# Optimization experiments

Hardware: AMD Instinct MI355X
Metric: run time of the kernel (lower is better)

The kernel has to match this reference:

```python
import jax, jax.numpy as jnp
import numpy as np

# hyperparameters (match init_kwargs)
LS = 0.2; GAMMA = 2.0; THING_W = 2.0; L_DB = 0.1; SIGMA = 0.05; TEMP = 0.1
L_DISTILL = 1.0; L_BPL = 0.5; L_ALIGN = 5.0; L_PROTO = 0.5; L_ENT = 0.3
L_IU = 0.5; L_IB = 0.5
MIN_PIX = 25; NUM_IDS = 24  # instance ids in [0, NUM_IDS)


def setup_inputs() -> dict:
    key = jax.random.key(0)
    k0, k1, k2, k3, k4 = jax.random.split(key, 5)
    B, C, H, W, D = 4, 27, 160, 160, 768
    return {
        "logits": jax.random.normal(k0, (B, C, H, W), jnp.float32),
        "cause_logits": jax.random.normal(k1, (B, C, H, W), jnp.float32),
        "dinov2_features": jax.random.normal(k2, (B, D, H, W), jnp.float32),
        "depth": jax.random.uniform(k3, (B, 1, H, W), jnp.float32),
        "instance_map": jax.random.randint(k4, (B, 1, H, W), 0, NUM_IDS),
    }


def _bce(x, y):
    x = jnp.clip(x, 1e-6, 1.0 - 1e-6)
    return -(y * jnp.log(x) + (1.0 - y) * jnp.log1p(-x)).mean()


def _forward(logits, cause_logits, dinov2_features, depth, instance_map):
    B, C, H, W = logits.shape
    logp = jax.nn.log_softmax(logits, axis=1)
    probs = jnp.exp(logp)

    # ---- distill: label-smoothed CE vs CAUSE hard labels, focal + thing + depth-boundary weights
    cause_labels = jnp.argmax(cause_logits, axis=1)  # (B,H,W)
    nll = -jnp.take_along_axis(logp, cause_labels[:, None], axis=1)[:, 0]  # (B,H,W)
    ce = (1.0 - LS) * nll + LS * (-logp.mean(axis=1))
    pt = jnp.exp(-jax.lax.stop_gradient(ce))
    w = (1.0 - pt) ** GAMMA
    thing = (cause_labels >= 11) & (cause_labels <= 18)
    w = jnp.where(thing, w * THING_W, w)
    gh = jnp.pad(jnp.abs(depth[:, :, 1:, :] - depth[:, :, :-1, :]), ((0, 0), (0, 0), (0, 1), (0, 0)))
    gw = jnp.pad(jnp.abs(depth[:, :, :, 1:] - depth[:, :, :, :-1]), ((0, 0), (0, 0), (0, 0), (0, 1)))
    gmag = (gh + gw)[:, 0]  # (B,H,W)
    gnorm = gmag / (gmag.mean() + 1e-6)
    w = w * (1.0 + L_DB * jnp.minimum(gnorm, 3.0))
    l_distill = (ce * w).mean()

    # ---- boundary preservation loss (CE re-weighted at pseudo-label boundaries)
    pl = jnp.pad(cause_labels, ((0, 0), (1, 1), (1, 1)), mode="edge")
    boundary = ((cause_labels != pl[:, 1:-1, 2:]) | (cause_labels != pl[:, 1:-1, :-2]) |
                (cause_labels != pl[:, 2:, 1:-1]) | (cause_labels != pl[:, :-2, 1:-1])).astype(jnp.float32)
    bsum = boundary.sum()
    l_bpl = jnp.where(bsum > 0, (ce * boundary).sum() / jnp.maximum(bsum, 1.0), 0.0)

    # ---- depth-boundary alignment
    two_s2 = 2.0 * SIGMA ** 2
    ddh = jnp.abs(depth[:, :, :, 1:] - depth[:, :, :, :-1])
    wh = jnp.exp(-(ddh ** 2) / two_s2)
    pdh = ((probs[:, :, :, 1:] - probs[:, :, :, :-1]) ** 2).sum(axis=1, keepdims=True)
    ddv = jnp.abs(depth[:, :, 1:, :] - depth[:, :, :-1, :])
    wv = jnp.exp(-(ddv ** 2) / two_s2)
    pdv = ((probs[:, :, 1:, :] - probs[:, :, :-1, :]) ** 2).sum(axis=1, keepdims=True)
    l_align = (wh * pdh).mean() + (wv * pdv).mean()

    # ---- feature prototype loss
    N = H * W
    probs_t = jax.nn.softmax(logits / TEMP, axis=1).reshape(B, C, N)   # (B,C,N)
    feats = dinov2_features.reshape(B, -1, N)                          # (B,D,N)
    protos = jnp.einsum("bdn,bcn->bdc", feats, probs_t)               # (B,D,C)
    wsum = probs_t.sum(axis=2)[:, None, :]                             # (B,1,C)
    protos = protos / (wsum + 1e-6)
    protos_n = protos / jnp.maximum(jnp.linalg.norm(protos, axis=1, keepdims=True), 1e-12)
    feats_n = feats / jnp.maximum(jnp.linalg.norm(feats, axis=1, keepdims=True), 1e-12)
    sim = jnp.einsum("bdc,bdn->bcn", protos_n, feats_n)               # (B,C,N)
    l_proto = -(probs_t * sim).sum() / (B * N)

    # ---- entropy loss
    l_ent = -(probs * logp).sum(axis=1).mean()

    # ---- instance boundary loss
    dh = jnp.abs(probs[:, :, 1:, :] - probs[:, :, :-1, :]).max(axis=1)
    dw = jnp.abs(probs[:, :, :, 1:] - probs[:, :, :, :-1]).max(axis=1)
    inst = instance_map[:, 0].astype(jnp.float32)
    th = (inst[:, 1:, :] != inst[:, :-1, :]).astype(jnp.float32)
    tw = (inst[:, :, 1:] != inst[:, :, :-1]).astype(jnp.float32)
    l_ib = (_bce(dh, th) + _bce(dw, tw)) / 2.0

    # ---- instance uniformity loss (vectorized segment reduce over instance ids)
    ids = instance_map[:, 0].reshape(B, N)                             # (B,N) int
    onehot = (ids[:, :, None] == jnp.arange(NUM_IDS)[None, None, :]).astype(jnp.float32)  # (B,N,K)
    counts = onehot.sum(axis=1)                                        # (B,K)
    pf = probs.reshape(B, C, N)
    s1 = jnp.einsum("bcn,bnk->bkc", pf, onehot)                       # per-id sum of probs
    s2 = jnp.einsum("bcn,bnk->bkc", pf * pf, onehot)                  # per-id sum of probs^2
    nc = jnp.maximum(counts, 1.0)[:, :, None]
    var = (s2 / nc - (s1 / nc) ** 2).mean(axis=2)                     # (B,K): mean over C of within-id variance
    valid = ((jnp.arange(NUM_IDS)[None, :] > 0) & (counts >= MIN_PIX)).astype(jnp.float32)
    l_iu = (var * valid).sum() / jnp.maximum(valid.sum(), 1.0)

    total = (L_DISTILL * l_distill + L_BPL * l_bpl + L_ALIGN * l_align +
             L_PROTO * l_proto + L_ENT * l_ent + L_IU * l_iu + L_IB * l_ib)
    return total


def reference(logits, cause_logits, dinov2_features, depth, instance_map):
    return _forward(logits, cause_logits, dinov2_features, depth, instance_map)
```

## Files before the change

kernel.cpp:

```cpp
#include <hip/hip_runtime.h>
#include <cstdint>
#include <cstddef>

#define BN 4
#define CC 27
#define HH 160
#define WW 160
#define HWp (HH*WW)
#define NPIX (BN*HWp)
#define DD 768
#define KK 24
#define NT 400
#define NTS 20
#define NSP 20
#define NPH (NTS/2)

#define OFF_ACC 0
#define OFF_S1 32
#define OFF_S2 (OFF_S1+2592)
#define OFF_CNT (OFF_S2+2592)
#define OFF_NSQ (OFF_CNT+96)
#define ZERO_N (OFF_NSQ+NPIX)
#define OFF_LAB ZERO_N
#define OFF_PROBS (OFF_LAB + NPIX/4)
#define OFF_PP (OFF_PROBS + BN*CC*HWp)
#define OFF_QP (OFF_PP + NSP*BN*CC*DD)
#define OFF_FBF (OFF_QP + NSP*BN*CC*DD)
#define OFF_WBF (OFF_FBF + (size_t)BN*6*NT*8192/4)

typedef __attribute__((ext_vector_type(4))) float f32x4;

__device__ __forceinline__ float wave_sum(float v) {
#pragma unroll
  for (int o = 32; o > 0; o >>= 1) v += __shfl_down(v, o, 64);
  return v;
}

__device__ __forceinline__ unsigned char f2fp8(float x) {
  return (unsigned char)(__builtin_amdgcn_cvt_pk_fp8_f32(x, x, 0, false) & 0xff);
}

__global__ void k_zero(float* __restrict__ w, int n) {
  int i = blockIdx.x * 256 + threadIdx.x;
  if (i < n) w[i] = 0.f;
}

__global__ void k_pre(const float* __restrict__ depth, const float* __restrict__ cl,
                      unsigned char* __restrict__ lab, float* __restrict__ acc) {
  int i = blockIdx.x * 256 + threadIdx.x;
  float g = 0.f;
  if (i < NPIX) {
    int b = i / HWp, r = i % HWp, h = r / WW, w = r % WW;
    const float* dp = depth + b * HWp;
    float d0 = dp[r];
    float gh = (h < HH-1) ? fabsf(dp[r+WW] - d0) : 0.f;
    float gw = (w < WW-1) ? fabsf(dp[r+1] - d0) : 0.f;
    g = gh + gw;
    const float* p = cl + (size_t)b * CC * HWp + r;
    float best = p[0]; int bi = 0;
#pragma unroll
    for (int c = 1; c < CC; ++c) {
      float v = p[(size_t)c * HWp];
      if (v > best) { best = v; bi = c; }
    }
    lab[i] = (unsigned char)bi;
  }
  __shared__ float red;
  if (threadIdx.x == 0) red = 0.f;
  __syncthreads();
  float s = wave_sum(g);
  if ((threadIdx.x & 63) == 0) atomicAdd(&red, s);
  __syncthreads();
  if (threadIdx.x == 0) atomicAdd(&acc[0], red);
}

__global__ void __launch_bounds__(256) k_fconv(const float* __restrict__ feats,
        unsigned char* __restrict__ fbf, float* __restrict__ nsq) {
  int t = threadIdx.x;
  int slab = blockIdx.x;
  int b = slab / (HWp / 1024);
  int px0 = (slab % (HWp / 1024)) * 1024;
  int d0 = blockIdx.y * (DD / 8);
  int p = px0 + 4 * t;
  int T = p >> 6, j = p & 63;
  const float* src = feats + ((size_t)b * DD + d0) * HWp + p;
  float n0 = 0.f, n1 = 0.f, n2 = 0.f, n3 = 0.f;
#pragma unroll 4
  for (int d = 0; d < DD / 8; ++d) {
    int dgl = d0 + d;
    float4 v = *(const float4*)(src + (size_t)d * HWp);
    n0 += v.x * v.x; n1 += v.y * v.y; n2 += v.z * v.z; n3 += v.w * v.w;
    int pk = __builtin_amdgcn_cvt_pk_fp8_f32(v.x, v.y, 0, false);
    pk = __builtin_amdgcn_cvt_pk_fp8_f32(v.z, v.w, pk, true);
    int dt = dgl >> 7, rin = dgl & 127;
    size_t addr = ((size_t)(b * 6 + dt) * NT + T) * 8192 + rin * 64
                + (((j >> 3) ^ (rin & 7)) * 8) + (j & 7);
    *(int*)&fbf[addr] = pk;
  }
  atomicAdd(&nsq[b * HWp + p + 0], n0);
  atomicAdd(&nsq[b * HWp + p + 1], n1);
  atomicAdd(&nsq[b * HWp + p + 2], n2);
  atomicAdd(&nsq[b * HWp + p + 3], n3);
}

__global__ void k_main(const float* __restrict__ logits, const float* __restrict__ depth,
                       const unsigned char* __restrict__ lab, const float* __restrict__ nsq,
                       float* __restrict__ probs, unsigned char* __restrict__ wbf,
                       float* __restrict__ acc) {
  int i = blockIdx.x * 256 + threadIdx.x;
  float c_dist = 0.f, c_bnum = 0.f, c_bcnt = 0.f, c_ent = 0.f;
  if (i < NPIX) {
    int b = i / HWp, r = i % HWp, h = r / WW, w = r % WW;
    const float* lg = logits + (size_t)b * CC * HWp + r;
    float x[CC];
    float m = -1e30f;
#pragma unroll
    for (int c = 0; c < CC; ++c) { x[c] = lg[(size_t)c * HWp]; m = fmaxf(m, x[c]); }
    float se = 0.f, sx = 0.f, set = 0.f;
#pragma unroll
    for (int c = 0; c < CC; ++c) {
      se += expf(x[c] - m);
      set += expf(10.f * (x[c] - m));
      sx += x[c];
    }
    float lse = logf(se);
    float inv_set = 1.f / set;
    float invn = 1.f / fmaxf(sqrtf(nsq[i]), 1e-12f);
    int l = lab[i];
    float xl = x[0];
    float ent = 0.f;
    float* pb = probs + (size_t)b * CC * HWp + r;
    int T = r >> 6, j = r & 63;
    unsigned char* wb = wbf + ((size_t)b * NT + T) * 4096;
#pragma unroll
    for (int c = 0; c < CC; ++c) {
      float lp = x[c] - m - lse;
      float p = expf(lp);
      pb[(size_t)c * HWp] = p;
      float ptc = expf(10.f * (x[c] - m)) * inv_set;
      wb[c * 64 + (((j >> 3) ^ (c & 7)) * 8) + (j & 7)] = f2fp8(ptc);
      int c2 = 32 + c;
      wb[c2 * 64 + (((j >> 3) ^ (c2 & 7)) * 8) + (j & 7)] = f2fp8(ptc * invn);
      ent -= p * lp;
      if (c == l) xl = x[c];
    }
    float nll = m + lse - xl;
    float ce = 0.8f * nll + 0.2f * (m + lse - sx * (1.f / CC));
    float ptf = expf(-ce);
    float wgt = (1.f - ptf) * (1.f - ptf);
    if (l >= 11 && l <= 18) wgt *= 2.f;
    const float* dp = depth + b * HWp;
    float d0 = dp[r];
    float gh = (h < HH-1) ? fabsf(dp[r+WW] - d0) : 0.f;
    float gw = (w < WW-1) ? fabsf(dp[r+1] - d0) : 0.f;
    float gmean = acc[0] * (1.f / NPIX);
    float gnorm = (gh + gw) / (gmean + 1e-6f);
    wgt *= 1.f + 0.1f * fminf(gnorm, 3.f);
    const unsigned char* lb = lab + b * HWp;
    int lL = lb[h*WW + (w>0 ? w-1 : w)];
    int lR = lb[h*WW + (w<WW-1 ? w+1 : w)];
    int lU = lb[(h>0 ? h-1 : h)*WW + w];
    int lD = lb[(h<HH-1 ? h+1 : h)*WW + w];
    float bnd = ((l != lL) | (l != lR) | (l != lU) | (l != lD)) ? 1.f : 0.f;
    c_dist = ce * wgt;
    c_bnum = ce * bnd;
    c_bcnt = bnd;
    c_ent = ent;
  }
  __shared__ float red[4];
  if (threadIdx.x < 4) red[threadIdx.x] = 0.f;
  __syncthreads();
  c_dist = wave_sum(c_dist); c_bnum = wave_sum(c_bnum);
  c_bcnt = wave_sum(c_bcnt); c_ent = wave_sum(c_ent);
  if ((threadIdx.x & 63) == 0) {
    atomicAdd(&red[0], c_dist); atomicAdd(&red[1], c_bnum);
    atomicAdd(&red[2], c_bcnt); atomicAdd(&red[3], c_ent);
  }
  __syncthreads();
  if (threadIdx.x == 0) {
    atomicAdd(&acc[1], red[0]); atomicAdd(&acc[2], red[1]);
    atomicAdd(&acc[3], red[2]); atomicAdd(&acc[4], red[3]);
  }
}

__global__ void __launch_bounds__(256) k_gemm(const unsigned char* __restrict__ fbf,
        const unsigned char* __restrict__ wbf,
        float* __restrict__ Pp, float* __restrict__ Qp) {
  __shared__ __align__(16) unsigned char As[3][2][8192];
  __shared__ __align__(16) unsigned char Ws[3][2][4096];
  int orig = blockIdx.x;
  int bx = (orig & 7) * 60 + (orig >> 3);
  int s  = bx % NSP;
  int dt = (bx / NSP) % 6;
  int b  = bx / (NSP * 6);
  int t = threadIdx.x;
  int wave = t >> 6, lane = t & 63;
  int g = lane >> 4, rr = lane & 15;
  f32x4 acc[2][4] = {};
  const unsigned char* Abase = fbf + ((size_t)(b*6+dt)*NT + s*NTS) * 8192;
  const unsigned char* Wbase = wbf + ((size_t)b*NT + s*NTS) * 4096;

#define STAGE2(ph, bufi) do { \
    _Pragma("unroll") \
    for (int c2_ = 0; c2_ < 2; ++c2_) { \
      const unsigned char* as_ = Abase + (size_t)((ph)*2 + c2_) * 8192; \
      const unsigned char* ws_ = Wbase + (size_t)((ph)*2 + c2_) * 4096; \
      _Pragma("unroll") \
      for (int i_ = 0; i_ < 2; ++i_) { \
        int off_ = wave*2048 + i_*1024; \
        __builtin_amdgcn_global_load_lds( \
          (const __attribute__((address_space(1))) void*)(as_ + off_ + lane*16), \
          (__attribute__((address_space(3))) void*)&As[bufi][c2_][off_], 16, 0, 0); \
      } \
      { \
        int off_ = wave*1024; \
        __builtin_amdgcn_global_load_lds( \
          (const __attribute__((address_space(1))) void*)(ws_ + off_ + lane*16), \
          (__attribute__((address_space(3))) void*)&Ws[bufi][c2_][off_], 16, 0, 0); \
      } \
    } \
  } while (0)

  STAGE2(0, 0);
  STAGE2(1, 1);
  int cur = 0;
  for (int ph = 0; ph < NPH; ++ph) {
    if (ph + 2 < NPH) {
      STAGE2(ph + 2, (cur + 2) % 3);
      asm volatile("s_waitcnt vmcnt(12)" ::: "memory");
    } else if (ph + 1 < NPH) {
      asm volatile("s_waitcnt vmcnt(6)" ::: "memory");
    } else {
      asm volatile("s_waitcnt vmcnt(0)" ::: "memory");
    }
    __builtin_amdgcn_s_barrier();
    __builtin_amdgcn_sched_barrier(0);
#pragma unroll
    for (int c2 = 0; c2 < 2; ++c2) {
#pragma unroll
      for (int ks = 0; ks < 2; ++ks) {
        long a[2]; long wf[4];
#pragma unroll
        for (int dd = 0; dd < 2; ++dd) {
          int row = (wave*2 + dd)*16 + rr;
          int ck = (ks*4 + g) ^ (row & 7);
          a[dd] = *(const long*)&As[cur][c2][row*64 + ck*8];
        }
#pragma unroll
        for (int ct = 0; ct < 4; ++ct) {
          int row = ct*16 + rr;
          int ck = (ks*4 + g) ^ (row & 7);
          wf[ct] = *(const long*)&Ws[cur][c2][row*64 + ck*8];
        }
#pragma unroll
        for (int dd = 0; dd < 2; ++dd)
#pragma unroll
          for (int ct = 0; ct < 4; ++ct)
            acc[dd][ct] = __builtin_amdgcn_mfma_f32_16x16x32_fp8_fp8(a[dd], wf[ct], acc[dd][ct], 0, 0, 0);
      }
    }
    __builtin_amdgcn_sched_barrier(0);
    __builtin_amdgcn_s_barrier();
    cur = (cur + 1) % 3;
  }
#undef STAGE2
#pragma unroll
  for (int dd = 0; dd < 2; ++dd) {
#pragma unroll
    for (int ct = 0; ct < 4; ++ct) {
      int cp = ct * 16 + rr;
      int d = dt * 128 + (wave * 2 + dd) * 16 + g * 4;
      f32x4 v = acc[dd][ct];
      if (cp < CC)
        *(f32x4*)&Pp[(((size_t)s * BN + b) * CC + cp) * DD + d] = v;
      else if (cp >= 32 && cp < 32 + CC)
        *(f32x4*)&Qp[(((size_t)s * BN + b) * CC + (cp - 32)) * DD + d] = v;
    }
  }
}

__global__ void k_tail(const float* __restrict__ probs, const float* __restrict__ depth,
                       const int* __restrict__ inst, float* __restrict__ acc,
                       float* __restrict__ s1g, float* __restrict__ s2g,
                       float* __restrict__ cntg) {
  __shared__ float ls1[4][KK*CC], ls2[4][KK*CC], lc[4][KK];
  int t = threadIdx.x; int wv = t >> 6;
  for (int idx = t; idx < 4*KK*CC; idx += 256) { (&ls1[0][0])[idx] = 0.f; (&ls2[0][0])[idx] = 0.f; }
  if (t < 4*KK) (&lc[0][0])[t] = 0.f;
  __syncthreads();
  int i = blockIdx.x * 256 + t;
  int b = i / HWp, r = i % HWp, h = r / WW, w = r % WW;
  const float* P = probs + (size_t)b * CC * HWp + r;
  const int* ip = inst + b * HWp;
  int id = ip[r];
  atomicAdd(&lc[wv][id], 1.f);
  bool hasR = (w < WW-1), hasD = (h < HH-1);
  float sh = 0.f, sv = 0.f, mh = 0.f, mw = 0.f;
#pragma unroll
  for (int c = 0; c < CC; ++c) {
    float p  = P[(size_t)c * HWp];
    atomicAdd(&ls1[wv][id*CC + c], p);
    atomicAdd(&ls2[wv][id*CC + c], p * p);
    float pr = hasR ? P[(size_t)c * HWp + 1]  : p;
    float pd = hasD ? P[(size_t)c * HWp + WW] : p;
    float dr = pr - p, dd = pd - p;
    sh += dr * dr; sv += dd * dd;
    mw = fmaxf(mw, fabsf(dr)); mh = fmaxf(mh, fabsf(dd));
  }
  float aH = 0.f, aV = 0.f, bh = 0.f, bw = 0.f;
  const float* dp = depth + b * HWp;
  float d0 = dp[r];
  if (hasR) {
    float ddh = dp[r+1] - d0;
    aH = expf(-(ddh*ddh) * 200.f) * sh;
    float y = (ip[r+1] != ip[r]) ? 1.f : 0.f;
    float xx = fminf(fmaxf(mw, 1e-6f), 1.f - 1e-6f);
    bw = -(y * logf(xx) + (1.f - y) * log1pf(-xx));
  }
  if (hasD) {
    float ddv = dp[r+WW] - d0;
    aV = expf(-(ddv*ddv) * 200.f) * sv;
    float y = (ip[r+WW] != ip[r]) ? 1.f : 0.f;
    float xx = fminf(fmaxf(mh, 1e-6f), 1.f - 1e-6f);
    bh = -(y * logf(xx) + (1.f - y) * log1pf(-xx));
  }
  __shared__ float red[4];
  if (t < 4) red[t] = 0.f;
  __syncthreads();
  aH = wave_sum(aH); aV = wave_sum(aV); bh = wave_sum(bh); bw = wave_sum(bw);
  if ((t & 63) == 0) {
    atomicAdd(&red[0], aH); atomicAdd(&red[1], aV);
    atomicAdd(&red[2], bh); atomicAdd(&red[3], bw);
  }
  __syncthreads();
  if (t == 0) {
    atomicAdd(&acc[5], red[0]); atomicAdd(&acc[6], red[1]);
    atomicAdd(&acc[7], red[2]); atomicAdd(&acc[8], red[3]);
  }
  for (int idx = t; idx < KK*CC; idx += 256) {
    atomicAdd(&s1g[b*KK*CC + idx], ls1[0][idx]+ls1[1][idx]+ls1[2][idx]+ls1[3][idx]);
    atomicAdd(&s2g[b*KK*CC + idx], ls2[0][idx]+ls2[1][idx]+ls2[2][idx]+ls2[3][idx]);
  }
  if (t < KK) atomicAdd(&cntg[b*KK + t], lc[0][t]+lc[1][t]+lc[2][t]+lc[3][t]);
}

__global__ void k_pfinal(const float* __restrict__ Pp, const float* __restrict__ Qp,
                         float* __restrict__ acc) {
  int bc = blockIdx.x;
  int b = bc / CC, c = bc % CC;
  float dot = 0.f, nsq = 0.f;
  for (int d = threadIdx.x; d < DD; d += 256) {
    float p = 0.f, q = 0.f;
#pragma unroll
    for (int s = 0; s < NSP; ++s) {
      size_t off = (((size_t)s * BN + b) * CC + c) * DD + d;
      p += Pp[off]; q += Qp[off];
    }
    dot += p * q; nsq += p * p;
  }
  __shared__ float red[2];
  if (threadIdx.x < 2) red[threadIdx.x] = 0.f;
  __syncthreads();
  dot = wave_sum(dot); nsq = wave_sum(nsq);
  if ((threadIdx.x & 63) == 0) { atomicAdd(&red[0], dot); atomicAdd(&red[1], nsq); }
  __syncthreads();
  if (threadIdx.x == 0) atomicAdd(&acc[9], red[0] / fmaxf(sqrtf(red[1]), 1e-12f));
}

__global__ void k_final(const float* __restrict__ s1g, const float* __restrict__ s2g,
                        const float* __restrict__ cntg, const float* __restrict__ acc,
                        float* __restrict__ out) {
  int t = threadIdx.x;
  float vsum = 0.f, vcnt = 0.f;
  if (t < BN*KK) {
    int k = t % KK;
    float count = cntg[t];
    float nc = fmaxf(count, 1.f);
    float var = 0.f;
#pragma unroll
    for (int c = 0; c < CC; ++c) {
      float m1 = s1g[t*CC + c] / nc;
      var += s2g[t*CC + c] / nc - m1 * m1;
    }
    var *= (1.f / CC);
    if (k > 0 && count >= 25.f) { vsum = var; vcnt = 1.f; }
  }
  __shared__ float red[2];
  if (t < 2) red[t] = 0.f;
  __syncthreads();
  vsum = wave_sum(vsum); vcnt = wave_sum(vcnt);
  if ((t & 63) == 0) { atomicAdd(&red[0], vsum); atomicAdd(&red[1], vcnt); }
  __syncthreads();
  if (t == 0) {
    float l_distill = acc[1] * (1.f / NPIX);
    float bcnt = acc[3];
    float l_bpl = (bcnt > 0.f) ? acc[2] / fmaxf(bcnt, 1.f) : 0.f;
    float l_align = acc[5] * (1.f / (BN*HH*(WW-1))) + acc[6] * (1.f / (BN*(HH-1)*WW));
    float l_ent = acc[4] * (1.f / NPIX);
    float l_ib = 0.5f * (acc[7] * (1.f / (BN*(HH-1)*WW)) + acc[8] * (1.f / (BN*HH*(WW-1))));
    float l_proto = -acc[9] * (1.f / NPIX);
    float l_iu = red[0] / fmaxf(red[1], 1.f);
    out[0] = 1.0f*l_distill + 0.5f*l_bpl + 5.0f*l_align + 0.5f*l_proto +
             0.3f*l_ent + 0.5f*l_iu + 0.5f*l_ib;
  }
}

extern "C" void kernel_launch(void* const* d_in, const int* in_sizes, int n_in,
                              void* d_out, int out_size, void* d_ws, size_t ws_size,
                              hipStream_t stream) {
  (void)in_sizes; (void)n_in; (void)out_size; (void)ws_size;
  const float* logits = (const float*)d_in[0];
  const float* cause  = (const float*)d_in[1];
  const float* feats  = (const float*)d_in[2];
  const float* depth  = (const float*)d_in[3];
  const int*   inst   = (const int*)d_in[4];
  float* ws = (float*)d_ws;
  float* acc = ws + OFF_ACC;
  float* s1  = ws + OFF_S1;
  float* s2  = ws + OFF_S2;
  float* cnt = ws + OFF_CNT;
  float* nsq = ws + OFF_NSQ;
  float* Pp  = ws + OFF_PP;
  float* Qp  = ws + OFF_QP;
  unsigned char* lab = (unsigned char*)(ws + OFF_LAB);
  float* probs = ws + OFF_PROBS;
  unsigned char* fbf = (unsigned char*)(ws + OFF_FBF);
  unsigned char* wbf = (unsigned char*)(ws + OFF_WBF);
  float* out = (float*)d_out;

  k_zero<<<(ZERO_N + 255) / 256, 256, 0, stream>>>(ws, ZERO_N);
  k_pre<<<NPIX / 256, 256, 0, stream>>>(depth, cause, lab, acc);
  k_fconv<<<dim3(NPIX / 1024, 8), 256, 0, stream>>>(feats, fbf, nsq);
  k_main<<<NPIX / 256, 256, 0, stream>>>(logits, depth, lab, nsq, probs, wbf, acc);
  k_gemm<<<BN * 6 * NSP, 256, 0, stream>>>(fbf, wbf, Pp, Qp);
  k_tail<<<NPIX / 256, 256, 0, stream>>>(probs, depth, inst, acc, s1, s2, cnt);
  k_pfinal<<<BN * CC, 256, 0, stream>>>(Pp, Qp, acc);
  k_final<<<1, 256, 0, stream>>>(s1, s2, cnt, acc, out);
}
```

Measured before the change: 211.2 us.

## Merge independent kernels by block range, store probs as bf16, drop nsq atomics

Fuses k_pre with k_fconv and k_gemm with k_tail into single launches that dispatch on block index, so independent work runs concurrently and launch gaps shrink. Per-slice squared norms are written to eight separate buffers and summed in k_main instead of using global atomics, which also removes nsq from the zeroed region. The probs intermediate is stored as bf16 to halve its write and read traffic. In exchange, the tail branch now reserves the GEMM's large shared-memory allocation, which may lower its occupancy, and bf16 probabilities add rounding to the variance and smoothness terms.

```diff
diff --git a/kernel.cpp b/kernel.cpp
--- a/kernel.cpp
+++ b/kernel.cpp
@@ -14,16 +14,18 @@
 #define NTS 20
 #define NSP 20
 #define NPH (NTS/2)
+#define GEMMB (BN*6*NSP)
+#define TAILB (NPIX/256)
 
 #define OFF_ACC 0
 #define OFF_S1 32
 #define OFF_S2 (OFF_S1+2592)
 #define OFF_CNT (OFF_S2+2592)
-#define OFF_NSQ (OFF_CNT+96)
-#define ZERO_N (OFF_NSQ+NPIX)
-#define OFF_LAB ZERO_N
+#define ZERO_N (OFF_CNT+96)
+#define OFF_NSQ8 ZERO_N
+#define OFF_LAB (OFF_NSQ8 + 8*NPIX)
 #define OFF_PROBS (OFF_LAB + NPIX/4)
-#define OFF_PP (OFF_PROBS + BN*CC*HWp)
+#define OFF_PP (OFF_PROBS + BN*CC*HWp/2)
 #define OFF_QP (OFF_PP + NSP*BN*CC*DD)
 #define OFF_FBF (OFF_QP + NSP*BN*CC*DD)
 #define OFF_WBF (OFF_FBF + (size_t)BN*6*NT*8192/4)
@@ -39,77 +41,87 @@
 __device__ __forceinline__ unsigned char f2fp8(float x) {
   return (unsigned char)(__builtin_amdgcn_cvt_pk_fp8_f32(x, x, 0, false) & 0xff);
 }
+__device__ __forceinline__ unsigned short f2bf(float x) {
+  unsigned u = __builtin_bit_cast(unsigned, x);
+  unsigned r = u + 0x7FFFu + ((u >> 16) & 1u);
+  return (unsigned short)(r >> 16);
+}
+__device__ __forceinline__ float bf2f(unsigned short u) {
+  unsigned v = ((unsigned)u) << 16;
+  return __builtin_bit_cast(float, v);
+}
 
 __global__ void k_zero(float* __restrict__ w, int n) {
   int i = blockIdx.x * 256 + threadIdx.x;
   if (i < n) w[i] = 0.f;
 }
 
-__global__ void k_pre(const float* __restrict__ depth, const float* __restrict__ cl,
-                      unsigned char* __restrict__ lab, float* __restrict__ acc) {
-  int i = blockIdx.x * 256 + threadIdx.x;
-  float g = 0.f;
-  if (i < NPIX) {
-    int b = i / HWp, r = i % HWp, h = r / WW, w = r % WW;
-    const float* dp = depth + b * HWp;
-    float d0 = dp[r];
-    float gh = (h < HH-1) ? fabsf(dp[r+WW] - d0) : 0.f;
-    float gw = (w < WW-1) ? fabsf(dp[r+1] - d0) : 0.f;
-    g = gh + gw;
-    const float* p = cl + (size_t)b * CC * HWp + r;
-    float best = p[0]; int bi = 0;
-#pragma unroll
-    for (int c = 1; c < CC; ++c) {
-      float v = p[(size_t)c * HWp];
-      if (v > best) { best = v; bi = c; }
-    }
-    lab[i] = (unsigned char)bi;
-  }
-  __shared__ float red;
-  if (threadIdx.x == 0) red = 0.f;
-  __syncthreads();
-  float s = wave_sum(g);
-  if ((threadIdx.x & 63) == 0) atomicAdd(&red, s);
-  __syncthreads();
-  if (threadIdx.x == 0) atomicAdd(&acc[0], red);
-}
-
-__global__ void __launch_bounds__(256) k_fconv(const float* __restrict__ feats,
-        unsigned char* __restrict__ fbf, float* __restrict__ nsq) {
+__global__ void __launch_bounds__(256) k_prefconv(const float* __restrict__ feats,
+        const float* __restrict__ depth, const float* __restrict__ cl,
+        unsigned char* __restrict__ fbf, float* __restrict__ nsq8,
+        unsigned char* __restrict__ lab, float* __restrict__ acc) {
   int t = threadIdx.x;
-  int slab = blockIdx.x;
-  int b = slab / (HWp / 1024);
-  int px0 = (slab % (HWp / 1024)) * 1024;
-  int d0 = blockIdx.y * (DD / 8);
-  int p = px0 + 4 * t;
-  int T = p >> 6, j = p & 63;
-  const float* src = feats + ((size_t)b * DD + d0) * HWp + p;
-  float n0 = 0.f, n1 = 0.f, n2 = 0.f, n3 = 0.f;
+  if (blockIdx.x < 800) {
+    int fcid = blockIdx.x;
+    int slab = fcid % 100;
+    int y = fcid / 100;
+    int b = slab / (HWp / 1024);
+    int px0 = (slab % (HWp / 1024)) * 1024;
+    int d0 = y * (DD / 8);
+    int p = px0 + 4 * t;
+    int T = p >> 6, j = p & 63;
+    const float* src = feats + ((size_t)b * DD + d0) * HWp + p;
+    float n0 = 0.f, n1 = 0.f, n2 = 0.f, n3 = 0.f;
 #pragma unroll 4
-  for (int d = 0; d < DD / 8; ++d) {
-    int dgl = d0 + d;
-    float4 v = *(const float4*)(src + (size_t)d * HWp);
-    n0 += v.x * v.x; n1 += v.y * v.y; n2 += v.z * v.z; n3 += v.w * v.w;
-    int pk = __builtin_amdgcn_cvt_pk_fp8_f32(v.x, v.y, 0, false);
-    pk = __builtin_amdgcn_cvt_pk_fp8_f32(v.z, v.w, pk, true);
-    int dt = dgl >> 7, rin = dgl & 127;
-    size_t addr = ((size_t)(b * 6 + dt) * NT + T) * 8192 + rin * 64
-                + (((j >> 3) ^ (rin & 7)) * 8) + (j & 7);
-    *(int*)&fbf[addr] = pk;
-  }
-  atomicAdd(&nsq[b * HWp + p + 0], n0);
-  atomicAdd(&nsq[b * HWp + p + 1], n1);
-  atomicAdd(&nsq[b * HWp + p + 2], n2);
-  atomicAdd(&nsq[b * HWp + p + 3], n3);
+    for (int d = 0; d < DD / 8; ++d) {
+      int dgl = d0 + d;
+      float4 v = *(const float4*)(src + (size_t)d * HWp);
+      n0 += v.x * v.x; n1 += v.y * v.y; n2 += v.z * v.z; n3 += v.w * v.w;
+      int pk = __builtin_amdgcn_cvt_pk_fp8_f32(v.x, v.y, 0, false);
+      pk = __builtin_amdgcn_cvt_pk_fp8_f32(v.z, v.w, pk, true);
+      int dt = dgl >> 7, rin = dgl & 127;
+      size_t addr = ((size_t)(b * 6 + dt) * NT + T) * 8192 + rin * 64
+                  + (((j >> 3) ^ (rin & 7)) * 8) + (j & 7);
+      *(int*)&fbf[addr] = pk;
+    }
+    float* nq = nsq8 + (size_t)y * NPIX + b * HWp + p;
+    nq[0] = n0; nq[1] = n1; nq[2] = n2; nq[3] = n3;
+  } else {
+    int i = (blockIdx.x - 800) * 256 + t;
+    float g = 0.f;
+    {
+      int b = i / HWp, r = i % HWp, h = r / WW, w = r % WW;
+      const float* dp = depth + b * HWp;
+      float d0 = dp[r];
+      float gh = (h < HH-1) ? fabsf(dp[r+WW] - d0) : 0.f;
+      float gw = (w < WW-1) ? fabsf(dp[r+1] - d0) : 0.f;
+      g = gh + gw;
+      const float* p = cl + (size_t)b * CC * HWp + r;
+      float best = p[0]; int bi = 0;
+#pragma unroll
+      for (int c = 1; c < CC; ++c) {
+        float v = p[(size_t)c * HWp];
+        if (v > best) { best = v; bi = c; }
+      }
+      lab[i] = (unsigned char)bi;
+    }
+    __shared__ float red;
+    if (t == 0) red = 0.f;
+    __syncthreads();
+    float s = wave_sum(g);
+    if ((t & 63) == 0) atomicAdd(&red, s);
+    __syncthreads();
+    if (t == 0) atomicAdd(&acc[0], red);
+  }
 }
 
 __global__ void k_main(const float* __restrict__ logits, const float* __restrict__ depth,
-                       const unsigned char* __restrict__ lab, const float* __restrict__ nsq,
-                       float* __restrict__ probs, unsigned char* __restrict__ wbf,
+                       const unsigned char* __restrict__ lab, const float* __restrict__ nsq8,
+                       unsigned short* __restrict__ probs, unsigned char* __restrict__ wbf,
                        float* __restrict__ acc) {
   int i = blockIdx.x * 256 + threadIdx.x;
   float c_dist = 0.f, c_bnum = 0.f, c_bcnt = 0.f, c_ent = 0.f;
-  if (i < NPIX) {
+  {
     int b = i / HWp, r = i % HWp, h = r / WW, w = r % WW;
     const float* lg = logits + (size_t)b * CC * HWp + r;
     float x[CC];
@@ -125,18 +137,21 @@
     }
     float lse = logf(se);
     float inv_set = 1.f / set;
-    float invn = 1.f / fmaxf(sqrtf(nsq[i]), 1e-12f);
+    float ns = 0.f;
+#pragma unroll
+    for (int y = 0; y < 8; ++y) ns += nsq8[(size_t)y * NPIX + i];
+    float invn = 1.f / fmaxf(sqrtf(ns), 1e-12f);
     int l = lab[i];
     float xl = x[0];
     float ent = 0.f;
-    float* pb = probs + (size_t)b * CC * HWp + r;
+    unsigned short* pb = probs + (size_t)b * CC * HWp + r;
     int T = r >> 6, j = r & 63;
     unsigned char* wb = wbf + ((size_t)b * NT + T) * 4096;
 #pragma unroll
     for (int c = 0; c < CC; ++c) {
       float lp = x[c] - m - lse;
       float p = expf(lp);
-      pb[(size_t)c * HWp] = p;
+      pb[(size_t)c * HWp] = f2bf(p);
       float ptc = expf(10.f * (x[c] - m)) * inv_set;
       wb[c * 64 + (((j >> 3) ^ (c & 7)) * 8) + (j & 7)] = f2fp8(ptc);
       int c2 = 32 + c;
@@ -183,22 +198,27 @@
   }
 }
 
-__global__ void __launch_bounds__(256) k_gemm(const unsigned char* __restrict__ fbf,
+__global__ void __launch_bounds__(256) k_gemmtail(const unsigned char* __restrict__ fbf,
         const unsigned char* __restrict__ wbf,
-        float* __restrict__ Pp, float* __restrict__ Qp) {
-  __shared__ __align__(16) unsigned char As[3][2][8192];
-  __shared__ __align__(16) unsigned char Ws[3][2][4096];
-  int orig = blockIdx.x;
-  int bx = (orig & 7) * 60 + (orig >> 3);
-  int s  = bx % NSP;
-  int dt = (bx / NSP) % 6;
-  int b  = bx / (NSP * 6);
+        float* __restrict__ Pp, float* __restrict__ Qp,
+        const unsigned short* __restrict__ probs, const float* __restrict__ depth,
+        const int* __restrict__ inst, float* __restrict__ acc,
+        float* __restrict__ s1g, float* __restrict__ s2g, float* __restrict__ cntg) {
+  __shared__ __align__(16) unsigned char smem[73728];
   int t = threadIdx.x;
-  int wave = t >> 6, lane = t & 63;
-  int g = lane >> 4, rr = lane & 15;
-  f32x4 acc[2][4] = {};
-  const unsigned char* Abase = fbf + ((size_t)(b*6+dt)*NT + s*NTS) * 8192;
-  const unsigned char* Wbase = wbf + ((size_t)b*NT + s*NTS) * 4096;
+  if (blockIdx.x < GEMMB) {
+    unsigned char (*As)[2][8192] = (unsigned char (*)[2][8192])smem;
+    unsigned char (*Ws)[2][4096] = (unsigned char (*)[2][4096])(smem + 49152);
+    int orig = blockIdx.x;
+    int bx = (orig & 7) * 60 + (orig >> 3);
+    int s  = bx % NSP;
+    int dt = (bx / NSP) % 6;
+    int b  = bx / (NSP * 6);
+    int wave = t >> 6, lane = t & 63;
+    int g = lane >> 4, rr = lane & 15;
+    f32x4 acc4[2][4] = {};
+    const unsigned char* Abase = fbf + ((size_t)(b*6+dt)*NT + s*NTS) * 8192;
+    const unsigned char* Wbase = wbf + ((size_t)b*NT + s*NTS) * 4096;
 
 #define STAGE2(ph, bufi) do { \
     _Pragma("unroll") \
@@ -221,127 +241,125 @@
     } \
   } while (0)
 
-  STAGE2(0, 0);
-  STAGE2(1, 1);
-  int cur = 0;
-  for (int ph = 0; ph < NPH; ++ph) {
-    if (ph + 2 < NPH) {
-      STAGE2(ph + 2, (cur + 2) % 3);
-      asm volatile("s_waitcnt vmcnt(12)" ::: "memory");
-    } else if (ph + 1 < NPH) {
-      asm volatile("s_waitcnt vmcnt(6)" ::: "memory");
-    } else {
-      asm volatile("s_waitcnt vmcnt(0)" ::: "memory");
-    }
-    __builtin_amdgcn_s_barrier();
-    __builtin_amdgcn_sched_barrier(0);
-#pragma unroll
-    for (int c2 = 0; c2 < 2; ++c2) {
-#pragma unroll
-      for (int ks = 0; ks < 2; ++ks) {
-        long a[2]; long wf[4];
-#pragma unroll
-        for (int dd = 0; dd < 2; ++dd) {
-          int row = (wave*2 + dd)*16 + rr;
-          int ck = (ks*4 + g) ^ (row & 7);
-          a[dd] = *(const long*)&As[cur][c2][row*64 + ck*8];
+    STAGE2(0, 0);
+    STAGE2(1, 1);
+    int cur = 0;
+    for (int ph = 0; ph < NPH; ++ph) {
+      if (ph + 2 < NPH) {
+        STAGE2(ph + 2, (cur + 2) % 3);
+        asm volatile("s_waitcnt vmcnt(12)" ::: "memory");
+      } else if (ph + 1 < NPH) {
+        asm volatile("s_waitcnt vmcnt(6)" ::: "memory");
+      } else {
+        asm volatile("s_waitcnt vmcnt(0)" ::: "memory");
+      }
+      __builtin_amdgcn_s_barrier();
+      __builtin_amdgcn_sched_barrier(0);
+#pragma unroll
+      for (int c2 = 0; c2 < 2; ++c2) {
+#pragma unroll
+        for (int ks = 0; ks < 2; ++ks) {
+          long a[2]; long wf[4];
+#pragma unroll
+          for (int dd = 0; dd < 2; ++dd) {
+            int row = (wave*2 + dd)*16 + rr;
+            int ck = (ks*4 + g) ^ (row & 7);
+            a[dd] = *(const long*)&As[cur][c2][row*64 + ck*8];
+          }
+#pragma unroll
+          for (int ct = 0; ct < 4; ++ct) {
+            int row = ct*16 + rr;
+            int ck = (ks*4 + g) ^ (row & 7);
+            wf[ct] = *(const long*)&Ws[cur][c2][row*64 + ck*8];
+          }
+#pragma unroll
+          for (int dd = 0; dd < 2; ++dd)
+#pragma unroll
+            for (int ct = 0; ct < 4; ++ct)
+              acc4[dd][ct] = __builtin_amdgcn_mfma_f32_16x16x32_fp8_fp8(a[dd], wf[ct], acc4[dd][ct], 0, 0, 0);
         }
-#pragma unroll
-        for (int ct = 0; ct < 4; ++ct) {
-          int row = ct*16 + rr;
-          int ck = (ks*4 + g) ^ (row & 7);
-          wf[ct] = *(const long*)&Ws[cur][c2][row*64 + ck*8];
-        }
-#pragma unroll
-        for (int dd = 0; dd < 2; ++dd)
-#pragma unroll
-          for (int ct = 0; ct < 4; ++ct)
-            acc[dd][ct] = __builtin_amdgcn_mfma_f32_16x16x32_fp8_fp8(a[dd], wf[ct], acc[dd][ct], 0, 0, 0);
       }
-    }
-    __builtin_amdgcn_sched_barrier(0);
-    __builtin_amdgcn_s_barrier();
-    cur = (cur + 1) % 3;
-  }
+      __builtin_amdgcn_sched_barrier(0);
+      __builtin_amdgcn_s_barrier();
+      cur = (cur + 1) % 3;
+    }
 #undef STAGE2
 #pragma unroll
-  for (int dd = 0; dd < 2; ++dd) {
-#pragma unroll
-    for (int ct = 0; ct < 4; ++ct) {
-      int cp = ct * 16 + rr;
-      int d = dt * 128 + (wave * 2 + dd) * 16 + g * 4;
-      f32x4 v = acc[dd][ct];
-      if (cp < CC)
-        *(f32x4*)&Pp[(((size_t)s * BN + b) * CC + cp) * DD + d] = v;
-      else if (cp >= 32 && cp < 32 + CC)
-        *(f32x4*)&Qp[(((size_t)s * BN + b) * CC + (cp - 32)) * DD + d] = v;
-    }
-  }
-}
-
-__global__ void k_tail(const float* __restrict__ probs, const float* __restrict__ depth,
-                       const int* __restrict__ inst, float* __restrict__ acc,
-                       float* __restrict__ s1g, float* __restrict__ s2g,
-                       float* __restrict__ cntg) {
-  __shared__ float ls1[4][KK*CC], ls2[4][KK*CC], lc[4][KK];
-  int t = threadIdx.x; int wv = t >> 6;
-  for (int idx = t; idx < 4*KK*CC; idx += 256) { (&ls1[0][0])[idx] = 0.f; (&ls2[0][0])[idx] = 0.f; }
-  if (t < 4*KK) (&lc[0][0])[t] = 0.f;
-  __syncthreads();
-  int i = blockIdx.x * 256 + t;
-  int b = i / HWp, r = i % HWp, h = r / WW, w = r % WW;
-  const float* P = probs + (size_t)b * CC * HWp + r;
-  const int* ip = inst + b * HWp;
-  int id = ip[r];
-  atomicAdd(&lc[wv][id], 1.f);
-  bool hasR = (w < WW-1), hasD = (h < HH-1);
-  float sh = 0.f, sv = 0.f, mh = 0.f, mw = 0.f;
-#pragma unroll
-  for (int c = 0; c < CC; ++c) {
-    float p  = P[(size_t)c * HWp];
-    atomicAdd(&ls1[wv][id*CC + c], p);
-    atomicAdd(&ls2[wv][id*CC + c], p * p);
-    float pr = hasR ? P[(size_t)c * HWp + 1]  : p;
-    float pd = hasD ? P[(size_t)c * HWp + WW] : p;
-    float dr = pr - p, dd = pd - p;
-    sh += dr * dr; sv += dd * dd;
-    mw = fmaxf(mw, fabsf(dr)); mh = fmaxf(mh, fabsf(dd));
-  }
-  float aH = 0.f, aV = 0.f, bh = 0.f, bw = 0.f;
-  const float* dp = depth + b * HWp;
-  float d0 = dp[r];
-  if (hasR) {
-    float ddh = dp[r+1] - d0;
-    aH = expf(-(ddh*ddh) * 200.f) * sh;
-    float y = (ip[r+1] != ip[r]) ? 1.f : 0.f;
-    float xx = fminf(fmaxf(mw, 1e-6f), 1.f - 1e-6f);
-    bw = -(y * logf(xx) + (1.f - y) * log1pf(-xx));
-  }
-  if (hasD) {
-    float ddv = dp[r+WW] - d0;
-    aV = expf(-(ddv*ddv) * 200.f) * sv;
-    float y = (ip[r+WW] != ip[r]) ? 1.f : 0.f;
-    float xx = fminf(fmaxf(mh, 1e-6f), 1.f - 1e-6f);
-    bh = -(y * logf(xx) + (1.f - y) * log1pf(-xx));
-  }
-  __shared__ float red[4];
-  if (t < 4) red[t] = 0.f;
-  __syncthreads();
-  aH = wave_sum(aH); aV = wave_sum(aV); bh = wave_sum(bh); bw = wave_sum(bw);
-  if ((t & 63) == 0) {
-    atomicAdd(&red[0], aH); atomicAdd(&red[1], aV);
-    atomicAdd(&red[2], bh); atomicAdd(&red[3], bw);
-  }
-  __syncthreads();
-  if (t == 0) {
-    atomicAdd(&acc[5], red[0]); atomicAdd(&acc[6], red[1]);
-    atomicAdd(&acc[7], red[2]); atomicAdd(&acc[8], red[3]);
-  }
-  for (int idx = t; idx < KK*CC; idx += 256) {
-    atomicAdd(&s1g[b*KK*CC + idx], ls1[0][idx]+ls1[1][idx]+ls1[2][idx]+ls1[3][idx]);
-    atomicAdd(&s2g[b*KK*CC + idx], ls2[0][idx]+ls2[1][idx]+ls2[2][idx]+ls2[3][idx]);
-  }
-  if (t < KK) atomicAdd(&cntg[b*KK + t], lc[0][t]+lc[1][t]+lc[2][t]+lc[3][t]);
+    for (int dd = 0; dd < 2; ++dd) {
+#pragma unroll
+      for (int ct = 0; ct < 4; ++ct) {
+        int cp = ct * 16 + rr;
+        int d = dt * 128 + (wave * 2 + dd) * 16 + g * 4;
+        f32x4 v = acc4[dd][ct];
+        if (cp < CC)
+          *(f32x4*)&Pp[(((size_t)s * BN + b) * CC + cp) * DD + d] = v;
+        else if (cp >= 32 && cp < 32 + CC)
+          *(f32x4*)&Qp[(((size_t)s * BN + b) * CC + (cp - 32)) * DD + d] = v;
+      }
+    }
+  } else {
+    float* ls1 = (float*)smem;
+    float* ls2 = ls1 + 4*KK*CC;
+    float* lc  = ls2 + 4*KK*CC;
+    float* red = lc + 4*KK;
+    int wv = t >> 6;
+    for (int idx = t; idx < 4*KK*CC; idx += 256) { ls1[idx] = 0.f; ls2[idx] = 0.f; }
+    if (t < 4*KK) lc[t] = 0.f;
+    if (t < 4) red[t] = 0.f;
+    __syncthreads();
+    int i = (blockIdx.x - GEMMB) * 256 + t;
+    int b = i / HWp, r = i % HWp, h = r / WW, w = r % WW;
+    const unsigned short* P = probs + (size_t)b * CC * HWp + r;
+    const int* ip = inst + b * HWp;
+    int id = ip[r];
+    atomicAdd(&lc[wv*KK + id], 1.f);
+    bool hasR = (w < WW-1), hasD = (h < HH-1);
+    float sh = 0.f, sv = 0.f, mh = 0.f, mw = 0.f;
+#pragma unroll
+    for (int c = 0; c < CC; ++c) {
+      float p  = bf2f(P[(size_t)c * HWp]);
+      atomicAdd(&ls1[(wv*KK + id)*CC + c], p);
+      atomicAdd(&ls2[(wv*KK + id)*CC + c], p * p);
+      float pr = hasR ? bf2f(P[(size_t)c * HWp + 1])  : p;
+      float pd = hasD ? bf2f(P[(size_t)c * HWp + WW]) : p;
+      float dr = pr - p, dd = pd - p;
+      sh += dr * dr; sv += dd * dd;
+      mw = fmaxf(mw, fabsf(dr)); mh = fmaxf(mh, fabsf(dd));
+    }
+    float aH = 0.f, aV = 0.f, bh = 0.f, bw = 0.f;
+    const float* dp = depth + b * HWp;
+    float d0 = dp[r];
+    if (hasR) {
+      float ddh = dp[r+1] - d0;
+      aH = expf(-(ddh*ddh) * 200.f) * sh;
+      float y = (ip[r+1] != ip[r]) ? 1.f : 0.f;
+      float xx = fminf(fmaxf(mw, 1e-6f), 1.f - 1e-6f);
+      bw = -(y * logf(xx) + (1.f - y) * log1pf(-xx));
+    }
+    if (hasD) {
+      float ddv = dp[r+WW] - d0;
+      aV = expf(-(ddv*ddv) * 200.f) * sv;
+      float y = (ip[r+WW] != ip[r]) ? 1.f : 0.f;
+      float xx = fminf(fmaxf(mh, 1e-6f), 1.f - 1e-6f);
+      bh = -(y * logf(xx) + (1.f - y) * log1pf(-xx));
+    }
+    __syncthreads();
+    aH = wave_sum(aH); aV = wave_sum(aV); bh = wave_sum(bh); bw = wave_sum(bw);
+    if ((t & 63) == 0) {
+      atomicAdd(&red[0], aH); atomicAdd(&red[1], aV);
+      atomicAdd(&red[2], bh); atomicAdd(&red[3], bw);
+    }
+    __syncthreads();
+    if (t == 0) {
+      atomicAdd(&acc[5], red[0]); atomicAdd(&acc[6], red[1]);
+      atomicAdd(&acc[7], red[2]); atomicAdd(&acc[8], red[3]);
+    }
+    for (int idx = t; idx < KK*CC; idx += 256) {
+      atomicAdd(&s1g[b*KK*CC + idx], ls1[idx]+ls1[KK*CC+idx]+ls1[2*KK*CC+idx]+ls1[3*KK*CC+idx]);
+      atomicAdd(&s2g[b*KK*CC + idx], ls2[idx]+ls2[KK*CC+idx]+ls2[2*KK*CC+idx]+ls2[3*KK*CC+idx]);
+    }
+    if (t < KK) atomicAdd(&cntg[b*KK + t], lc[t]+lc[KK+t]+lc[2*KK+t]+lc[3*KK+t]);
+  }
 }
 
 __global__ void k_pfinal(const float* __restrict__ Pp, const float* __restrict__ Qp,
@@ -419,21 +437,20 @@
   float* s1  = ws + OFF_S1;
   float* s2  = ws + OFF_S2;
   float* cnt = ws + OFF_CNT;
-  float* nsq = ws + OFF_NSQ;
+  float* nsq8 = ws + OFF_NSQ8;
   float* Pp  = ws + OFF_PP;
   float* Qp  = ws + OFF_QP;
   unsigned char* lab = (unsigned char*)(ws + OFF_LAB);
-  float* probs = ws + OFF_PROBS;
+  unsigned short* probs = (unsigned short*)(ws + OFF_PROBS);
   unsigned char* fbf = (unsigned char*)(ws + OFF_FBF);
   unsigned char* wbf = (unsigned char*)(ws + OFF_WBF);
   float* out = (float*)d_out;
 
   k_zero<<<(ZERO_N + 255) / 256, 256, 0, stream>>>(ws, ZERO_N);
-  k_pre<<<NPIX / 256, 256, 0, stream>>>(depth, cause, lab, acc);
-  k_fconv<<<dim3(NPIX / 1024, 8), 256, 0, stream>>>(feats, fbf, nsq);
-  k_main<<<NPIX / 256, 256, 0, stream>>>(logits, depth, lab, nsq, probs, wbf, acc);
-  k_gemm<<<BN * 6 * NSP, 256, 0, stream>>>(fbf, wbf, Pp, Qp);
-  k_tail<<<NPIX / 256, 256, 0, stream>>>(probs, depth, inst, acc, s1, s2, cnt);
+  k_prefconv<<<1200, 256, 0, stream>>>(feats, depth, cause, fbf, nsq8, lab, acc);
+  k_main<<<NPIX / 256, 256, 0, stream>>>(logits, depth, lab, nsq8, probs, wbf, acc);
+  k_gemmtail<<<GEMMB + TAILB, 256, 0, stream>>>(fbf, wbf, Pp, Qp, probs, depth, inst,
+                                                acc, s1, s2, cnt);
   k_pfinal<<<BN * CC, 256, 0, stream>>>(Pp, Qp, acc);
   k_final<<<1, 256, 0, stream>>>(s1, s2, cnt, acc, out);
 }
```

Measured after the change: 194.7 us. 7.8% less time.
